# Performance work log

Hardware: AMD Instinct MI355X
Metric: run time of the kernel (lower is better)

Reference implementation:

```python
import jax, jax.numpy as jnp
import numpy as np

B, NV, HID, TDIM = 1024, 256, 256, 128
NODE_IN = 2 + 4 + TDIM  # coords + pos_enc(4) + time_emb


def _sinusoidal_pos_emb(t, dim):
    # standard SinusoidalPosEmb: cat(sin, cos) of t * exp(-i*log(1e4)/(half-1))
    half = dim // 2
    freqs = jnp.exp(-np.log(10000.0) * jnp.arange(half, dtype=t.dtype) / (half - 1))
    ang = t[:, None] * freqs[None, :]
    return jnp.concatenate([jnp.sin(ang), jnp.cos(ang)], axis=-1)  # [B, dim]


def setup_inputs() -> dict:
    key = jax.random.key(0)
    ks = jax.random.split(key, 10)
    s = lambda fan_in: 1.0 / np.sqrt(fan_in)
    return {
        "x": jax.random.normal(ks[0], (B, NV * 2), dtype=jnp.float32),
        "t": jax.random.uniform(ks[1], (B,), dtype=jnp.float32) * 1000.0,
        "time_w": jax.random.normal(ks[2], (TDIM, TDIM), dtype=jnp.float32) * s(TDIM),
        "time_b": jnp.zeros((TDIM,), dtype=jnp.float32),
        "W0": jax.random.normal(ks[3], (NODE_IN, HID), dtype=jnp.float32) * s(NODE_IN),
        "b0": jnp.zeros((HID,), dtype=jnp.float32),
        "W1": jax.random.normal(ks[4], (HID, HID), dtype=jnp.float32) * s(HID),
        "b1": jnp.zeros((HID,), dtype=jnp.float32),
        "W2": jax.random.normal(ks[5], (HID, HID), dtype=jnp.float32) * s(HID),
        "b2": jnp.zeros((HID,), dtype=jnp.float32),
    }


def reference(x, t, time_w, time_b, W0, b0, W1, b1, W2, b2):
    Bsz, D = x.shape
    n = D // 2
    coords = x.reshape(Bsz, n, 2)  # [B, n, 2]

    # cycle positional features (pos_enc_dim=4): sin/cos of vertex angle + 2nd harmonic
    pos = jnp.arange(n, dtype=x.dtype)
    theta = (2.0 * jnp.pi) * pos / n
    pe = jnp.stack([jnp.sin(theta), jnp.cos(theta), jnp.sin(2.0 * theta), jnp.cos(2.0 * theta)], axis=-1)
    pe = jnp.broadcast_to(pe[None], (Bsz, n, 4))

    # time MLP: SinusoidalPosEmb -> Linear -> SiLU, broadcast to every node of the graph
    temb = jax.nn.silu(_sinusoidal_pos_emb(t, time_w.shape[0]) @ time_w + time_b)  # [B, TDIM]
    temb = jnp.broadcast_to(temb[:, None, :], (Bsz, n, temb.shape[-1]))

    h = jnp.concatenate([coords, pe, temb], axis=-1)  # [B, n, NODE_IN]

    # GCN layers over cycle adjacency with self-loops, symmetric-normalized (deg=3 -> 1/3).
    # Cycle structure: neighbors are prev/next vertex within each polygon -> jnp.roll on axis 1.
    for W, b in ((W0, b0), (W1, b1), (W2, b2)):
        s = h @ W + b  # support = x W + b
        agg = (s + jnp.roll(s, 1, axis=1) + jnp.roll(s, -1, axis=1)) / 3.0
        h = jax.nn.silu(agg)

    # mean pooling per graph (scatter_mean over graph_index == mean over vertex axis here)
    return h.mean(axis=1)  # [B, HID]
```

## Files before the change

kernel.cpp:

```cpp
#include <hip/hip_runtime.h>
#include <cstdint>

typedef __attribute__((ext_vector_type(8)))  short bf16x8;
typedef __attribute__((ext_vector_type(16))) float f32x16;
typedef __attribute__((ext_vector_type(4)))  int   i32x4;

__device__ __forceinline__ unsigned short f2bf(float x) {
  unsigned u = __float_as_uint(x);
  u += 0x7fffu + ((u >> 16) & 1u);
  return (unsigned short)(u >> 16);
}
__device__ __forceinline__ unsigned pk2bf(float lo, float hi) {
#if defined(__has_builtin)
#if __has_builtin(__builtin_amdgcn_cvt_pk_bf16_f32)
  auto v = __builtin_amdgcn_cvt_pk_bf16_f32(lo, hi);
  unsigned u; __builtin_memcpy(&u, &v, 4); return u;
#else
  return ((unsigned)f2bf(hi) << 16) | (unsigned)f2bf(lo);
#endif
#else
  return ((unsigned)f2bf(hi) << 16) | (unsigned)f2bf(lo);
#endif
}
__device__ __forceinline__ float silu_f(float v) {
  return v * __builtin_amdgcn_rcpf(1.0f + __expf(-v));
}

__device__ __forceinline__ float xchg32(float A, float B, int q) {
#if defined(__has_builtin)
#if __has_builtin(__builtin_amdgcn_permlane32_swap)
  auto r = __builtin_amdgcn_permlane32_swap(__float_as_uint(A), __float_as_uint(B),
                                            false, false);
  return __uint_as_float(q ? r[0] : r[1]);
#else
  return __shfl_xor(q ? A : B, 32);
#endif
#else
  return __shfl_xor(q ? A : B, 32);
#endif
}

__global__ void pack_kernel(const float* __restrict__ W0, const float* __restrict__ W1,
                            const float* __restrict__ W2,
                            unsigned short* __restrict__ packW) {
  __shared__ float ldsF[16][257];
  const int s = blockIdx.x, tid = threadIdx.x;
  const float* W; int KT, kmax, base, kt;
  if (s < 9)       { W = W0; KT = 9;  kmax = 134; base = 0;      kt = s; }
  else if (s < 25) { W = W1; KT = 16; kmax = 256; base = 36864;  kt = s - 9; }
  else             { W = W2; KT = 16; kmax = 256; base = 102400; kt = s - 25; }
  const int k0 = kt * 16;
#pragma unroll
  for (int i = 0; i < 8; ++i) {
    const int idx = i * 512 + tid;
    const int kl = idx >> 8, col = idx & 255;
    const int kg = k0 + kl;
    ldsF[kl][col] = (kg < kmax) ? W[kg * 256 + col] * 0.33333334f : 0.0f;
  }
  __syncthreads();
  const int g = tid >> 7, t = (tid >> 6) & 1, lane = tid & 63;
  const int col = g * 64 + t * 32 + (lane & 31);
  const int kb = 8 * (lane >> 5);
  unsigned u0 = pk2bf(ldsF[kb + 0][col], ldsF[kb + 1][col]);
  unsigned u1 = pk2bf(ldsF[kb + 2][col], ldsF[kb + 3][col]);
  unsigned u2 = pk2bf(ldsF[kb + 4][col], ldsF[kb + 5][col]);
  unsigned u3 = pk2bf(ldsF[kb + 6][col], ldsF[kb + 7][col]);
  unsigned short* dst = packW + base + g * (KT * 1024) + t * (KT * 512) + kt * 512 + lane * 8;
  i32x4 v = { (int)u0, (int)u1, (int)u2, (int)u3 };
  *(i32x4*)dst = v;
}


template <int ELAYER, bool DF, bool DL>
__device__ __forceinline__ void epi_pair(
    const int p, const f32x16* accEpi, const int q,
    const float recvI0, const float recvI1, const float recvX,
    const float extP, const float extN,
    const int epiSub, unsigned short* __restrict__ hbuf,
    const int* rowAddr, float& psum) {
  const int t = p >> 3, rp = (p & 7) * 2;
  const float mid = accEpi[t][rp] + accEpi[t][rp + 1];
  float prev, next;
  if (rp > 0) prev = accEpi[t][rp - 1];
  else        prev = q ? (t ? recvI1 : recvI0) : (t ? recvX : extP);
  if (rp < 14) next = accEpi[t][rp + 2];
  else         next = q ? (t ? extN : recvX) : (t ? recvI1 : recvI0);
  const float y0 = silu_f(prev + mid);
  const float y1 = silu_f(mid + next);
  const bool c0 = !(DF && t == 0 && rp == 0 && q == 0);
  const bool c1 = !(DL && t == 1 && rp == 14 && q == 1);
  if constexpr (ELAYER == 2) {
    if (c0) psum += y0;
    if (c1) psum += y1;
  } else {
    const unsigned u = pk2bf(y0, y1);
    char* bp = (char*)hbuf + (2 * epiSub + t) * 16384;
    if (c0) *(unsigned short*)(bp + rowAddr[rp])     = (unsigned short)u;
    if (c1) *(unsigned short*)(bp + rowAddr[rp + 1]) = (unsigned short)(u >> 16);
  }
}

template <int KT, int ELAYER, bool DOEPI, bool DF, bool DL>
__device__ __forceinline__ void fblock(
    unsigned short* __restrict__ hbuf, const int readSub, const int epiSub,
    const bf16x8* Bf, const int q, const int c, const float bias3,
    f32x16* accOut, const f32x16* accEpi,
    const float extP, const float extN,
    const int* rowAddr, float& psum) {
  float recvI0 = 0.f, recvI1 = 0.f, recvX = 0.f;
  if constexpr (DOEPI) {
    recvI0 = xchg32(accEpi[0][0],  accEpi[0][15], q);
    recvI1 = xchg32(accEpi[1][0],  accEpi[1][15], q);
    recvX  = xchg32(accEpi[0][15], accEpi[1][0],  q);
  }
#pragma unroll
  for (int t2 = 0; t2 < 2; ++t2)
#pragma unroll
    for (int j = 0; j < 16; ++j) accOut[t2][j] = bias3;
  const unsigned short* rb = hbuf + readSub * 16384 + c * 256;
  bf16x8 a0 = *(const bf16x8*)(rb + ((q ^ c) * 8));
  bf16x8 a1 = *(const bf16x8*)(rb + ((q ^ c) * 8) + 8192);
#pragma unroll
  for (int kt = 0; kt < KT; ++kt) {
    const bf16x8 u0 = a0, u1 = a1;
    if (kt + 1 < KT) {
      const unsigned short* nb = rb + (((2 * (kt + 1) + q) ^ c) * 8);
      a0 = *(const bf16x8*)(nb);
      a1 = *(const bf16x8*)(nb + 8192);
    }
    accOut[0] = __builtin_amdgcn_mfma_f32_32x32x16_bf16(u0, Bf[kt], accOut[0], 0, 0, 0);
    accOut[1] = __builtin_amdgcn_mfma_f32_32x32x16_bf16(u1, Bf[kt], accOut[1], 0, 0, 0);
    if constexpr (DOEPI) {
#pragma unroll
      for (int p = (kt * 16) / KT; p < ((kt + 1) * 16) / KT; ++p)
        epi_pair<ELAYER, DF, DL>(p, accEpi, q, recvI0, recvI1, recvX, extP, extN,
                                 epiSub, hbuf, rowAddr, psum);
    }
  }
}

template <int ELAYER>
__device__ __forceinline__ void epi_only(
    const f32x16* accEpi, const int q, const float extP, const float extN,
    const int epiSub, unsigned short* __restrict__ hbuf,
    const int* rowAddr, float& psum) {
  const float recvI0 = xchg32(accEpi[0][0],  accEpi[0][15], q);
  const float recvI1 = xchg32(accEpi[1][0],  accEpi[1][15], q);
  const float recvX  = xchg32(accEpi[0][15], accEpi[1][0],  q);
#pragma unroll
  for (int p = 0; p < 16; ++p)
    epi_pair<ELAYER, false, false>(p, accEpi, q, recvI0, recvI1, recvX, extP, extN,
                                   epiSub, hbuf, rowAddr, psum);
}

template <int ELAYER>
__device__ __forceinline__ void defer_last(
    const f32x16* accEpi, const float accNew00, const int epiSub,
    const int q, unsigned short* __restrict__ hbuf,
    const int* rowAddr, float& psum) {
  const float recv = xchg32(0.f, accNew00, q);
  const float y = silu_f(accEpi[1][14] + accEpi[1][15] + recv);
  if (q) {
    if constexpr (ELAYER == 2) psum += y;
    else *(unsigned short*)((char*)hbuf + (2 * epiSub + 1) * 16384 + rowAddr[15]) = f2bf(y);
  }
}

template <int ELAYER>
__device__ __forceinline__ void fix_node0(
    const float s255src, const float sv0, const float sv1,
    const int q, unsigned short* __restrict__ hbuf,
    const int* rowAddr, float& psum) {
  const float recv = xchg32(s255src, 0.f, q);
  const float y = silu_f(recv + sv0 + sv1);
  if (!q) {
    if constexpr (ELAYER == 2) psum += y;
    else *(unsigned short*)((char*)hbuf + rowAddr[0]) = f2bf(y);
  }
}

__global__ __launch_bounds__(512, 1) void poly_kernel(
    const float* __restrict__ x, const float* __restrict__ t,
    const float* __restrict__ tw, const float* __restrict__ tb,
    const unsigned short* __restrict__ packW,
    const float* __restrict__ B0, const float* __restrict__ B1,
    const float* __restrict__ B2, float* __restrict__ out) {
  __shared__ __align__(16) unsigned short hbuf[65536];
  __shared__ __align__(16) unsigned short tmpl[160];

  const int tid = threadIdx.x;
  const int w = tid >> 6, lane = tid & 63, q = lane >> 5, c = lane & 31;
  const int b = blockIdx.x;

  {
    float* scr = (float*)hbuf;
    if (tid < 128) {
      const float tv = t[b];
      const int i = tid & 63;
      const float f = expf(-0.14619588396823767f * (float)i);
      const float ang = tv * f;
      scr[tid] = (tid < 64) ? sinf(ang) : cosf(ang);
    }
    __syncthreads();
    {
      const int j = tid & 127, p = tid >> 7;
      float a = 0.f;
#pragma unroll 8
      for (int kk = 0; kk < 32; ++kk) a += scr[p * 32 + kk] * tw[(p * 32 + kk) * 128 + j];
      scr[128 + tid] = a;
    }
    __syncthreads();
    if (tid < 128) {
      const float a = tb[tid] + scr[128 + tid] + scr[256 + tid] + scr[384 + tid] + scr[512 + tid];
      tmpl[6 + tid] = f2bf(silu_f(a));
      if (tid < 6)  tmpl[tid] = 0;
      if (tid < 26) tmpl[134 + tid] = 0;
    }
    __syncthreads();
  }

  const unsigned short* pL0 = packW + (w >> 1) * (9 * 1024) + (w & 1) * (9 * 512);
  const unsigned short* pL1 = packW + 36864 + (w >> 1) * (16 * 1024) + (w & 1) * (16 * 512);
  const unsigned short* pL2 = packW + 102400 + (w >> 1) * (16 * 1024) + (w & 1) * (16 * 512);
  bf16x8 Bf[16];
#pragma unroll
  for (int kt = 0; kt < 9; ++kt) Bf[kt] = *(const bf16x8*)(pL0 + kt * 512 + lane * 8);
  const float b30 = B0[w * 32 + c] * 0.33333334f;
  const float b31 = B1[w * 32 + c] * 0.33333334f;
  const float b32 = B2[w * 32 + c] * 0.33333334f;

  float initL0;
  {
    f32x16 Ct;
#pragma unroll
    for (int j = 0; j < 16; ++j) Ct[j] = 0.f;
#pragma unroll
    for (int kt = 0; kt < 9; ++kt) {
      const bf16x8 at = *(const bf16x8*)(tmpl + kt * 16 + q * 8);
      Ct = __builtin_amdgcn_mfma_f32_32x32x16_bf16(at, Bf[kt], Ct, 0, 0, 0);
    }
    initL0 = Ct[0] + b30;
  }

  {
    const int node = tid >> 1, sl = tid & 1;
    i32x4 d = {0, 0, 0, 0};
    if (sl == 0) {
      const float2 xy = ((const float2*)x)[b * 256 + node];
      const float th = 0.024543692605870074f * (float)node;
      d.x = (int)pk2bf(xy.x, xy.y);
      d.y = (int)pk2bf(sinf(th), cosf(th));
      d.z = (int)pk2bf(sinf(2.f * th), cosf(2.f * th));
    }
    const int m = (node & 3) + 8 * ((node >> 2) & 3) + 4 * ((node >> 4) & 1);
    const int R = (node & ~31) | m;
    *(i32x4*)(hbuf + R * 256 + ((sl ^ m) * 8)) = d;
  }

  int rowAddr[16];
  const int slotW = 4 * w + (c >> 3), offW = (c & 7) * 2;
#pragma unroll
  for (int r = 0; r < 16; ++r) {
    const int row = (r & 3) + 8 * (r >> 2) + 4 * q;
    rowAddr[r] = row * 512 + ((slotW ^ row) * 16) + offW;
  }
  __syncthreads();

  f32x16 accA[2], accB[2];
  float psum = 0.f, sv0, sv1, extP, extN;

  fblock<1, 0, false, false, false>(hbuf, 0, 0, Bf, q, c, initL0, accA, accA, 0.f, 0.f, rowAddr, psum);
  sv0 = accA[0][0]; sv1 = accA[0][1];
  __syncthreads();
  fblock<1, 0, true, true, true>(hbuf, 1, 0, Bf, q, c, initL0, accB, accA, 0.f, 0.f, rowAddr, psum);
  defer_last<0>(accA, accB[0][0], 0, q, hbuf, rowAddr, psum);
  extP = xchg32(accA[1][15], 0.f, q);
  __syncthreads();
  fblock<1, 0, true, false, true>(hbuf, 2, 1, Bf, q, c, initL0, accA, accB, extP, 0.f, rowAddr, psum);
  defer_last<0>(accB, accA[0][0], 1, q, hbuf, rowAddr, psum);
  extP = xchg32(accB[1][15], 0.f, q);
  __syncthreads();
  fblock<1, 0, true, false, true>(hbuf, 3, 2, Bf, q, c, initL0, accB, accA, extP, 0.f, rowAddr, psum);
  defer_last<0>(accA, accB[0][0], 2, q, hbuf, rowAddr, psum);
  fix_node0<0>(accB[1][15], sv0, sv1, q, hbuf, rowAddr, psum);
  extP = xchg32(accA[1][15], 0.f, q);
  extN = xchg32(0.f, sv0, q);
#pragma unroll
  for (int kt = 0; kt < 16; ++kt) Bf[kt] = *(const bf16x8*)(pL1 + kt * 512 + lane * 8);
  __syncthreads();

  fblock<16, 0, true, false, false>(hbuf, 0, 3, Bf, q, c, b31, accA, accB, extP, extN, rowAddr, psum);
  sv0 = accA[0][0]; sv1 = accA[0][1];
  __syncthreads();
  fblock<16, 1, true, true, true>(hbuf, 1, 0, Bf, q, c, b31, accB, accA, 0.f, 0.f, rowAddr, psum);
  defer_last<1>(accA, accB[0][0], 0, q, hbuf, rowAddr, psum);
  extP = xchg32(accA[1][15], 0.f, q);
  __syncthreads();
  fblock<16, 1, true, false, true>(hbuf, 2, 1, Bf, q, c, b31, accA, accB, extP, 0.f, rowAddr, psum);
  defer_last<1>(accB, accA[0][0], 1, q, hbuf, rowAddr, psum);
  extP = xchg32(accB[1][15], 0.f, q);
  __syncthreads();
  fblock<16, 1, true, false, true>(hbuf, 3, 2, Bf, q, c, b31, accB, accA, extP, 0.f, rowAddr, psum);
  defer_last<1>(accA, accB[0][0], 2, q, hbuf, rowAddr, psum);
  fix_node0<1>(accB[1][15], sv0, sv1, q, hbuf, rowAddr, psum);
  extP = xchg32(accA[1][15], 0.f, q);
  extN = xchg32(0.f, sv0, q);
#pragma unroll
  for (int kt = 0; kt < 16; ++kt) Bf[kt] = *(const bf16x8*)(pL2 + kt * 512 + lane * 8);
  __syncthreads();

  fblock<16, 1, true, false, false>(hbuf, 0, 3, Bf, q, c, b32, accA, accB, extP, extN, rowAddr, psum);
  sv0 = accA[0][0]; sv1 = accA[0][1];
  __syncthreads();
  fblock<16, 2, true, true, true>(hbuf, 1, 0, Bf, q, c, b32, accB, accA, 0.f, 0.f, rowAddr, psum);
  defer_last<2>(accA, accB[0][0], 0, q, hbuf, rowAddr, psum);
  extP = xchg32(accA[1][15], 0.f, q);
  fblock<16, 2, true, false, true>(hbuf, 2, 1, Bf, q, c, b32, accA, accB, extP, 0.f, rowAddr, psum);
  defer_last<2>(accB, accA[0][0], 1, q, hbuf, rowAddr, psum);
  extP = xchg32(accB[1][15], 0.f, q);
  fblock<16, 2, true, false, true>(hbuf, 3, 2, Bf, q, c, b32, accB, accA, extP, 0.f, rowAddr, psum);
  defer_last<2>(accA, accB[0][0], 2, q, hbuf, rowAddr, psum);
  fix_node0<2>(accB[1][15], sv0, sv1, q, hbuf, rowAddr, psum);
  extP = xchg32(accA[1][15], 0.f, q);
  extN = xchg32(0.f, sv0, q);
  epi_only<2>(accB, q, extP, extN, 3, hbuf, rowAddr, psum);

  const float s2 = psum + xchg32(psum, psum, q);
  if (q == 0) out[b * 256 + w * 32 + c] = s2 * (1.0f / 256.0f);
}

extern "C" void kernel_launch(void* const* d_in, const int* in_sizes, int n_in,
                              void* d_out, int out_size, void* d_ws, size_t ws_size,
                              hipStream_t stream) {
  const float* x  = (const float*)d_in[0];
  const float* t  = (const float*)d_in[1];
  const float* tw = (const float*)d_in[2];
  const float* tb = (const float*)d_in[3];
  const float* W0 = (const float*)d_in[4];
  const float* b0 = (const float*)d_in[5];
  const float* W1 = (const float*)d_in[6];
  const float* b1 = (const float*)d_in[7];
  const float* W2 = (const float*)d_in[8];
  const float* b2 = (const float*)d_in[9];

  unsigned short* packW = (unsigned short*)d_ws;
  float* out = (float*)d_out;

  pack_kernel<<<41, 512, 0, stream>>>(W0, W1, W2, packW);
  poly_kernel<<<1024, 512, 0, stream>>>(x, t, tw, tb, packW, b0, b1, b2, out);
}
```

Measured before the change: 176.3 us.

## Fuse weight packing into main kernel and deepen LDS prefetch in MMA loop

```diff
diff --git a/kernel.cpp b/kernel.cpp
--- a/kernel.cpp
+++ b/kernel.cpp
@@ -40,34 +40,26 @@
 #endif
 }
 
-__global__ void pack_kernel(const float* __restrict__ W0, const float* __restrict__ W1,
-                            const float* __restrict__ W2,
-                            unsigned short* __restrict__ packW) {
-  __shared__ float ldsF[16][257];
-  const int s = blockIdx.x, tid = threadIdx.x;
-  const float* W; int KT, kmax, base, kt;
-  if (s < 9)       { W = W0; KT = 9;  kmax = 134; base = 0;      kt = s; }
-  else if (s < 25) { W = W1; KT = 16; kmax = 256; base = 36864;  kt = s - 9; }
-  else             { W = W2; KT = 16; kmax = 256; base = 102400; kt = s - 25; }
-  const int k0 = kt * 16;
-#pragma unroll
-  for (int i = 0; i < 8; ++i) {
-    const int idx = i * 512 + tid;
-    const int kl = idx >> 8, col = idx & 255;
-    const int kg = k0 + kl;
-    ldsF[kl][col] = (kg < kmax) ? W[kg * 256 + col] * 0.33333334f : 0.0f;
-  }
-  __syncthreads();
-  const int g = tid >> 7, t = (tid >> 6) & 1, lane = tid & 63;
-  const int col = g * 64 + t * 32 + (lane & 31);
-  const int kb = 8 * (lane >> 5);
-  unsigned u0 = pk2bf(ldsF[kb + 0][col], ldsF[kb + 1][col]);
-  unsigned u1 = pk2bf(ldsF[kb + 2][col], ldsF[kb + 3][col]);
-  unsigned u2 = pk2bf(ldsF[kb + 4][col], ldsF[kb + 5][col]);
-  unsigned u3 = pk2bf(ldsF[kb + 6][col], ldsF[kb + 7][col]);
-  unsigned short* dst = packW + base + g * (KT * 1024) + t * (KT * 512) + kt * 512 + lane * 8;
-  i32x4 v = { (int)u0, (int)u1, (int)u2, (int)u3 };
-  *(i32x4*)dst = v;
+__device__ __forceinline__ bf16x8 loadW3(const float* __restrict__ Wp,
+                                         const int kbase, const int col) {
+  float f[8];
+#pragma unroll
+  for (int j = 0; j < 8; ++j) f[j] = Wp[(kbase + j) * 256 + col] * 0.33333334f;
+  i32x4 v = { (int)pk2bf(f[0], f[1]), (int)pk2bf(f[2], f[3]),
+              (int)pk2bf(f[4], f[5]), (int)pk2bf(f[6], f[7]) };
+  return __builtin_bit_cast(bf16x8, v);
+}
+__device__ __forceinline__ bf16x8 loadW3m(const float* __restrict__ Wp,
+                                          const int kbase, const int col, const int kmax) {
+  float f[8];
+#pragma unroll
+  for (int j = 0; j < 8; ++j) {
+    const int k = kbase + j;
+    f[j] = (k < kmax) ? Wp[k * 256 + col] * 0.33333334f : 0.f;
+  }
+  i32x4 v = { (int)pk2bf(f[0], f[1]), (int)pk2bf(f[2], f[3]),
+              (int)pk2bf(f[4], f[5]), (int)pk2bf(f[6], f[7]) };
+  return __builtin_bit_cast(bf16x8, v);
 }
 
 
@@ -118,15 +110,20 @@
 #pragma unroll
     for (int j = 0; j < 16; ++j) accOut[t2][j] = bias3;
   const unsigned short* rb = hbuf + readSub * 16384 + c * 256;
-  bf16x8 a0 = *(const bf16x8*)(rb + ((q ^ c) * 8));
-  bf16x8 a1 = *(const bf16x8*)(rb + ((q ^ c) * 8) + 8192);
+  bf16x8 pa[2], pb[2];
+  pa[0] = *(const bf16x8*)(rb + ((q ^ c) * 8));
+  pb[0] = *(const bf16x8*)(rb + ((q ^ c) * 8) + 8192);
+  if (KT > 1) {
+    pa[1] = *(const bf16x8*)(rb + (((2 + q) ^ c) * 8));
+    pb[1] = *(const bf16x8*)(rb + (((2 + q) ^ c) * 8) + 8192);
+  }
 #pragma unroll
   for (int kt = 0; kt < KT; ++kt) {
-    const bf16x8 u0 = a0, u1 = a1;
-    if (kt + 1 < KT) {
-      const unsigned short* nb = rb + (((2 * (kt + 1) + q) ^ c) * 8);
-      a0 = *(const bf16x8*)(nb);
-      a1 = *(const bf16x8*)(nb + 8192);
+    const bf16x8 u0 = pa[kt & 1], u1 = pb[kt & 1];
+    if (kt + 2 < KT) {
+      const unsigned short* nb = rb + (((2 * (kt + 2) + q) ^ c) * 8);
+      pa[kt & 1] = *(const bf16x8*)(nb);
+      pb[kt & 1] = *(const bf16x8*)(nb + 8192);
     }
     accOut[0] = __builtin_amdgcn_mfma_f32_32x32x16_bf16(u0, Bf[kt], accOut[0], 0, 0, 0);
     accOut[1] = __builtin_amdgcn_mfma_f32_32x32x16_bf16(u1, Bf[kt], accOut[1], 0, 0, 0);
@@ -182,15 +179,17 @@
 __global__ __launch_bounds__(512, 1) void poly_kernel(
     const float* __restrict__ x, const float* __restrict__ t,
     const float* __restrict__ tw, const float* __restrict__ tb,
-    const unsigned short* __restrict__ packW,
-    const float* __restrict__ B0, const float* __restrict__ B1,
-    const float* __restrict__ B2, float* __restrict__ out) {
+    const float* __restrict__ W0, const float* __restrict__ B0,
+    const float* __restrict__ W1, const float* __restrict__ B1,
+    const float* __restrict__ W2, const float* __restrict__ B2,
+    float* __restrict__ out) {
   __shared__ __align__(16) unsigned short hbuf[65536];
   __shared__ __align__(16) unsigned short tmpl[160];
 
   const int tid = threadIdx.x;
   const int w = tid >> 6, lane = tid & 63, q = lane >> 5, c = lane & 31;
   const int b = blockIdx.x;
+  const int col = w * 32 + c;
 
   {
     float* scr = (float*)hbuf;
@@ -219,15 +218,13 @@
     __syncthreads();
   }
 
-  const unsigned short* pL0 = packW + (w >> 1) * (9 * 1024) + (w & 1) * (9 * 512);
-  const unsigned short* pL1 = packW + 36864 + (w >> 1) * (16 * 1024) + (w & 1) * (16 * 512);
-  const unsigned short* pL2 = packW + 102400 + (w >> 1) * (16 * 1024) + (w & 1) * (16 * 512);
   bf16x8 Bf[16];
 #pragma unroll
-  for (int kt = 0; kt < 9; ++kt) Bf[kt] = *(const bf16x8*)(pL0 + kt * 512 + lane * 8);
-  const float b30 = B0[w * 32 + c] * 0.33333334f;
-  const float b31 = B1[w * 32 + c] * 0.33333334f;
-  const float b32 = B2[w * 32 + c] * 0.33333334f;
+  for (int kt = 0; kt < 8; ++kt) Bf[kt] = loadW3(W0, kt * 16 + 8 * q, col);
+  Bf[8] = loadW3m(W0, 128 + 8 * q, col, 134);
+  const float b30 = B0[col] * 0.33333334f;
+  const float b31 = B1[col] * 0.33333334f;
+  const float b32 = B2[col] * 0.33333334f;
 
   float initL0;
   {
@@ -281,12 +278,12 @@
   extP = xchg32(accB[1][15], 0.f, q);
   __syncthreads();
   fblock<1, 0, true, false, true>(hbuf, 3, 2, Bf, q, c, initL0, accB, accA, extP, 0.f, rowAddr, psum);
+#pragma unroll
+  for (int kt = 0; kt < 16; ++kt) Bf[kt] = loadW3(W1, kt * 16 + 8 * q, col);
   defer_last<0>(accA, accB[0][0], 2, q, hbuf, rowAddr, psum);
   fix_node0<0>(accB[1][15], sv0, sv1, q, hbuf, rowAddr, psum);
   extP = xchg32(accA[1][15], 0.f, q);
   extN = xchg32(0.f, sv0, q);
-#pragma unroll
-  for (int kt = 0; kt < 16; ++kt) Bf[kt] = *(const bf16x8*)(pL1 + kt * 512 + lane * 8);
   __syncthreads();
 
   fblock<16, 0, true, false, false>(hbuf, 0, 3, Bf, q, c, b31, accA, accB, extP, extN, rowAddr, psum);
@@ -301,12 +298,12 @@
   extP = xchg32(accB[1][15], 0.f, q);
   __syncthreads();
   fblock<16, 1, true, false, true>(hbuf, 3, 2, Bf, q, c, b31, accB, accA, extP, 0.f, rowAddr, psum);
+#pragma unroll
+  for (int kt = 0; kt < 16; ++kt) Bf[kt] = loadW3(W2, kt * 16 + 8 * q, col);
   defer_last<1>(accA, accB[0][0], 2, q, hbuf, rowAddr, psum);
   fix_node0<1>(accB[1][15], sv0, sv1, q, hbuf, rowAddr, psum);
   extP = xchg32(accA[1][15], 0.f, q);
   extN = xchg32(0.f, sv0, q);
-#pragma unroll
-  for (int kt = 0; kt < 16; ++kt) Bf[kt] = *(const bf16x8*)(pL2 + kt * 512 + lane * 8);
   __syncthreads();
 
   fblock<16, 1, true, false, false>(hbuf, 0, 3, Bf, q, c, b32, accA, accB, extP, extN, rowAddr, psum);
@@ -326,7 +323,7 @@
   epi_only<2>(accB, q, extP, extN, 3, hbuf, rowAddr, psum);
 
   const float s2 = psum + xchg32(psum, psum, q);
-  if (q == 0) out[b * 256 + w * 32 + c] = s2 * (1.0f / 256.0f);
+  if (q == 0) out[b * 256 + col] = s2 * (1.0f / 256.0f);
 }
 
 extern "C" void kernel_launch(void* const* d_in, const int* in_sizes, int n_in,
@@ -342,10 +339,7 @@
   const float* b1 = (const float*)d_in[7];
   const float* W2 = (const float*)d_in[8];
   const float* b2 = (const float*)d_in[9];
-
-  unsigned short* packW = (unsigned short*)d_ws;
   float* out = (float*)d_out;
 
-  pack_kernel<<<41, 512, 0, stream>>>(W0, W1, W2, packW);
-  poly_kernel<<<1024, 512, 0, stream>>>(x, t, tw, tb, packW, b0, b1, b2, out);
-}
+  poly_kernel<<<1024, 512, 0, stream>>>(x, t, tw, tb, W0, b0, W1, b1, W2, b2, out);
+}
```

Measured after the change: 246.0 us. +39.5%, slower.
